# Optimization experiments

Hardware: AMD Instinct MI355X
Metric: run time of the kernel (lower is better)

Reference implementation:

```python
import jax, jax.numpy as jnp
import numpy as np
from jax import lax

LEVEL = 128  # level_num

def _bn(x, g, b, m, v):
    # inference-mode BatchNorm, channel axis = 1
    sh = (1, -1) + (1,) * (x.ndim - 2)
    return (x - m.reshape(sh)) * (g.reshape(sh) * lax.rsqrt(v.reshape(sh) + 1e-5)) + b.reshape(sh)

def _leaky(a):
    return jnp.where(a > 0, a, 0.01 * a)

def _l2n(a):
    return a / jnp.maximum(jnp.linalg.norm(a, axis=1, keepdims=True), 1e-12)

def _resize_bilinear_ac(x, oh, ow):
    # bilinear, align_corners=True, NCHW
    n, c, h, w = x.shape
    ys = jnp.linspace(0.0, h - 1.0, oh)
    xs = jnp.linspace(0.0, w - 1.0, ow)
    y0 = jnp.floor(ys).astype(jnp.int32)
    x0 = jnp.floor(xs).astype(jnp.int32)
    y1 = jnp.minimum(y0 + 1, h - 1)
    x1 = jnp.minimum(x0 + 1, w - 1)
    wy = (ys - y0)[:, None]
    wx = (xs - x0)[None, :]
    Y0, Y1, X0, X1 = y0[:, None], y1[:, None], x0[None, :], x1[None, :]
    return (x[:, :, Y0, X0] * (1 - wy) * (1 - wx) + x[:, :, Y0, X1] * (1 - wy) * wx
            + x[:, :, Y1, X0] * wy * (1 - wx) + x[:, :, Y1, X1] * wy * wx)

def _forward(x, conv1_w, bn1_g, bn1_b, bn1_m, bn1_v, conv2_w, f1_w, f2_w, f2_g, f2_b, f2_m, f2_v,
             out1_w, out1_g, out1_b, out1_m, out1_v, k_w, q_w, v_w, out_w, out_g, out_b, out_m, out_v):
    # conv1: 3x3 conv + BN + LeakyReLU
    y = lax.conv_general_dilated(x, conv1_w, (1, 1), 'SAME', dimension_numbers=('NCHW', 'OIHW', 'NCHW'))
    y = _leaky(_bn(y, bn1_g, bn1_b, bn1_m, bn1_v))
    # conv2: 1x1 conv, 256->128
    x2 = jnp.einsum('nchw,oc->nohw', y, conv2_w)
    N, C, H, W = x2.shape  # C = 128
    x_ave = x2.mean(axis=(2, 3), keepdims=True)  # [N,C,1,1]
    cos = (_l2n(x_ave) * _l2n(x2)).sum(1)        # [N,H,W]
    sh, sw = H // 3, W // 3
    L = sh * sw
    # H,W divisible by 3 -> adaptive_avg_pool2d is identity
    cs = cos.reshape(N, 3, sh, 3, sw).transpose(0, 1, 3, 2, 4).reshape(N, 9, L).transpose(0, 2, 1)  # [N,L,9]
    # LBP bit packing vs center (index 4); weight 0 at index 4 (strict > gives 0 there)
    bits = (cs > cs[:, :, 4:5]).astype(x.dtype)
    wts = jnp.array([1, 2, 4, 8, 0, 16, 32, 64, 128], dtype=x.dtype)
    code = (bits * wts).sum(-1)  # [N,L]
    mn = code.min(-1, keepdims=True)
    mx = code.max(-1, keepdims=True)
    code = (code - mn) / (mx - mn)
    cmin = code.min(-1, keepdims=True)
    cmax = code.max(-1, keepdims=True)
    qlv = (2 * jnp.arange(LEVEL, dtype=x.dtype) + 1) / (2 * LEVEL) * (cmax - cmin) + cmin  # [N,LEVEL]
    inter = (qlv[:, 1] - qlv[:, 0])[:, None, None]  # [N,1,1]
    quant = 1 - jnp.abs(qlv[:, None, :] - code[:, :, None])  # [N,L,LEVEL]
    quant = jnp.where(quant > 1 - inter, quant, 0.0)
    sta = quant.sum(1)                                       # [N,LEVEL]
    sta = sta / sta.sum(-1, keepdims=True)
    sta2 = jnp.stack([qlv, sta], axis=1)                     # [N,2,LEVEL]
    h1 = _leaky(jnp.einsum('ncl,oc->nol', sta2, f1_w))       # f1: 2->64
    h2 = jax.nn.relu(_bn(jnp.einsum('ncl,oc->nol', h1, f2_w), f2_g, f2_b, f2_m, f2_v))  # f2: 64->128
    xa = jnp.broadcast_to(x_ave[:, :, 0, 0][:, :, None], (N, C, LEVEL))
    s = jnp.concatenate([h2, xa], axis=1)                    # [N,256,LEVEL]
    s = jax.nn.relu(_bn(jnp.einsum('ncl,oc->nol', s, out1_w), out1_g, out1_b, out1_m, out1_v))
    k = jnp.einsum('ncl,oc->nol', s, k_w)
    q = jnp.einsum('ncl,oc->nol', s, q_w)
    v = jnp.einsum('ncl,oc->nol', s, v_w)
    w = jax.nn.softmax(jnp.einsum('ncl,ncm->nlm', k, q), axis=-1)  # bmm(k^T, q)
    f = jnp.einsum('nlm,ncm->ncl', w, v)                            # bmm(w, v^T) then transpose
    f = jax.nn.relu(_bn(jnp.einsum('ncl,oc->nol', f, out_w), out_g, out_b, out_m, out_v))
    out = jnp.einsum('ncl,npl->ncp', f, quant).reshape(N, 256, sh, sh)  # bmm(f, quant^T)
    return _resize_bilinear_ac(out, H, W)

def setup_inputs() -> dict:
    key = jax.random.key(0)
    ks = jax.random.split(key, 16)
    f32 = jnp.float32
    def nrm(k, shape, s=0.05):
        return s * jax.random.normal(k, shape, f32)
    def bnp(k, c):
        k1, k2, k3, k4 = jax.random.split(k, 4)
        return (1.0 + 0.1 * jax.random.normal(k1, (c,), f32),
                0.1 * jax.random.normal(k2, (c,), f32),
                0.1 * jax.random.normal(k3, (c,), f32),
                jax.random.uniform(k4, (c,), f32, 0.5, 1.5))
    d = {}
    d['x'] = jax.random.normal(ks[0], (32, 512, 48, 48), f32)
    d['conv1_w'] = nrm(ks[1], (256, 512, 3, 3))
    d['bn1_g'], d['bn1_b'], d['bn1_m'], d['bn1_v'] = bnp(ks[2], 256)
    d['conv2_w'] = nrm(ks[3], (128, 256))
    d['f1_w'] = nrm(ks[4], (64, 2), 0.3)
    d['f2_w'] = nrm(ks[5], (128, 64), 0.1)
    d['f2_g'], d['f2_b'], d['f2_m'], d['f2_v'] = bnp(ks[6], 128)
    d['out1_w'] = nrm(ks[7], (256, 256))
    d['out1_g'], d['out1_b'], d['out1_m'], d['out1_v'] = bnp(ks[8], 256)
    d['k_w'] = nrm(ks[9], (256, 256))
    d['q_w'] = nrm(ks[10], (256, 256))
    d['v_w'] = nrm(ks[11], (256, 256))
    d['out_w'] = nrm(ks[12], (256, 256))
    d['out_g'], d['out_b'], d['out_m'], d['out_v'] = bnp(ks[13], 256)
    return d

def reference(x, conv1_w, bn1_g, bn1_b, bn1_m, bn1_v, conv2_w, f1_w, f2_w, f2_g, f2_b, f2_m, f2_v,
              out1_w, out1_g, out1_b, out1_m, out1_v, k_w, q_w, v_w, out_w, out_g, out_b, out_m, out_v):
    return _forward(x, conv1_w, bn1_g, bn1_b, bn1_m, bn1_v, conv2_w, f1_w, f2_w, f2_g, f2_b, f2_m, f2_v,
                    out1_w, out1_g, out1_b, out1_m, out1_v, k_w, q_w, v_w, out_w, out_g, out_b, out_m, out_v)
```

## Files before the change

kernel.cpp:

```cpp
#include <hip/hip_runtime.h>
#include <math.h>

#define N_IMG 32
#define P2304 2304
#define CIN 512
#define CMID 256
#define C2 128
#define LEV 128

typedef _Float16 half8 __attribute__((ext_vector_type(8)));
typedef float f32x16 __attribute__((ext_vector_type(16)));
typedef unsigned short u16;
typedef unsigned int u32;

__device__ __forceinline__ float wredSum(float v){
#pragma unroll
  for (int o = 32; o > 0; o >>= 1) v += __shfl_down(v, o, 64);
  return v;
}
__device__ __forceinline__ float wredMax(float v){
#pragma unroll
  for (int o = 32; o > 0; o >>= 1) v = fmaxf(v, __shfl_down(v, o, 64));
  return v;
}
__device__ __forceinline__ float wredMin(float v){
#pragma unroll
  for (int o = 32; o > 0; o >>= 1) v = fminf(v, __shfl_down(v, o, 64));
  return v;
}

__device__ __forceinline__ void gll16(const void* g, void* l){
  __builtin_amdgcn_global_load_lds(
      (const __attribute__((address_space(1))) void*)g,
      (__attribute__((address_space(3))) void*)l, 16, 0, 0);
}

__global__ void prep_w1_kernel(const float* __restrict__ w1,
                               uint4* __restrict__ Wh, uint4* __restrict__ Wl){
  int fid = blockIdx.x * 256 + threadIdx.x;
  int lam = fid & 63;
  int c32 = (fid >> 6) & 3;
  int cot = (fid >> 8) & 1;
  int kt  = fid >> 9;
  int co = cot * 128 + c32 * 32 + (lam & 31);
  half8 vh, vl;
#pragma unroll
  for (int j = 0; j < 8; ++j){
    int k = kt * 16 + ((lam >> 5) << 3) + j;
    int r = k >> 9;
    int ci = k & 511;
    float v = w1[co * (CIN * 9) + ci * 9 + r];
    _Float16 h = (_Float16)v;
    vh[j] = h;
    vl[j] = (_Float16)((v - (float)h) * 2048.0f);
  }
  Wh[fid] = *(uint4*)&vh;
  Wl[fid] = *(uint4*)&vl;
}

__global__ void prep_w2_kernel(const float* __restrict__ w2,
                               uint4* __restrict__ Wh, uint4* __restrict__ Wl){
  int fid = blockIdx.x * 256 + threadIdx.x;
  int lam = fid & 63;
  int c32 = (fid >> 6) & 3;
  int kt  = fid >> 8;
  int co = c32 * 32 + (lam & 31);
  half8 vh, vl;
#pragma unroll
  for (int j = 0; j < 8; ++j){
    int k = kt * 16 + ((lam >> 5) << 3) + j;
    float v = w2[co * CMID + k];
    _Float16 h = (_Float16)v;
    vh[j] = h;
    vl[j] = (_Float16)((v - (float)h) * 2048.0f);
  }
  Wh[fid] = *(uint4*)&vh;
  Wl[fid] = *(uint4*)&vl;
}

__global__ void prep_bn_kernel(const float* __restrict__ g1, const float* __restrict__ b1,
                               const float* __restrict__ m1, const float* __restrict__ v1,
                               float* __restrict__ s1, float* __restrict__ t1){
  int c = threadIdx.x;
  float s = g1[c] * (1.0f / sqrtf(v1[c] + 1e-5f));
  s1[c] = s;
  t1[c] = b1[c] - m1[c] * s;
}

__global__ void prep_x_kernel(const float* __restrict__ x,
                              u16* __restrict__ xh, u16* __restrict__ xl,
                              int n0){
  __shared__ float tile[128 * 49];
  const int t = threadIdx.x;
  const int b = blockIdx.x;
  const int n_loc = b / 50;
  const int hp = b - n_loc * 50;
  const int n = n0 + n_loc;
  const int h = hp - 1;
  const bool vrow = (h >= 0) && (h < 48);
  const size_t base_n = (size_t)n_loc * 1280000;
  for (int cc = 0; cc < 4; ++cc){
    if (vrow){
      const float* src = x + (((size_t)n * 512 + cc * 128) * 48 + h) * 48;
#pragma unroll
      for (int i = 0; i < 24; ++i){
        int idx = t + 256 * i;
        int w = idx % 48;
        int c = idx / 48;
        tile[c * 49 + w] = src[(size_t)c * 2304 + w];
      }
    }
    __syncthreads();
    for (int i = 0; i < 13; ++i){
      int idx = t + 256 * i;
      if (idx < 3200){
        int ck_loc = idx / 400;
        int rem = idx - ck_loc * 400;
        int wp = rem >> 3;
        int clp = rem & 7;
        int w = wp - 1;
        int c_loc = ck_loc * 16 + clp * 2;
        float v0 = 0.f, v1 = 0.f;
        if (vrow && (unsigned)w < 48u){
          v0 = tile[c_loc * 49 + w];
          v1 = tile[(c_loc + 1) * 49 + w];
        }
        _Float16 h0 = (_Float16)v0, h1 = (_Float16)v1;
        _Float16 l0 = (_Float16)((v0 - (float)h0) * 2048.0f);
        _Float16 l1 = (_Float16)((v1 - (float)h1) * 2048.0f);
        union { _Float16 hh[2]; u32 uu; } ph, pl;
        ph.hh[0] = h0; ph.hh[1] = h1;
        pl.hh[0] = l0; pl.hh[1] = l1;
        size_t off = base_n + ((size_t)(cc * 8 + ck_loc) * 2500
                               + hp * 50 + wp) * 16 + clp * 2;
        *(u32*)(xh + off) = ph.uu;
        *(u32*)(xl + off) = pl.uu;
      }
    }
    __syncthreads();
  }
}

#define COMPUTE_M(CUR, KF)                                                    \
  {                                                                           \
    const int ct0 = (g & 1) * 2, pt0 = (g >> 1) * 2;                          \
    half8 fAh[2], fAl[2], fBh[2], fBl[2];                                     \
    _Pragma("unroll")                                                         \
    for (int a = 0; a < 2; ++a){                                              \
      fAh[a] = *(half8*)&Abuf[CUR][KF][0][(ct0 + a) * 512 + lam * 8];         \
      fAl[a] = *(half8*)&Abuf[CUR][KF][1][(ct0 + a) * 512 + lam * 8];         \
      fBh[a] = *(half8*)&Bbuf[CUR][KF][0][(pt0 + a) * 512 + lam * 8];         \
      fBl[a] = *(half8*)&Bbuf[CUR][KF][1][(pt0 + a) * 512 + lam * 8];         \
    }                                                                         \
    _Pragma("unroll")                                                         \
    for (int a = 0; a < 2; ++a)                                               \
      _Pragma("unroll")                                                       \
      for (int b = 0; b < 2; ++b){                                            \
        acc_hh[a][b] = __builtin_amdgcn_mfma_f32_32x32x16_f16(                \
            fAh[a], fBh[b], acc_hh[a][b], 0, 0, 0);                           \
        acc_x[a][b] = __builtin_amdgcn_mfma_f32_32x32x16_f16(                 \
            fAh[a], fBl[b], acc_x[a][b], 0, 0, 0);                            \
        acc_x[a][b] = __builtin_amdgcn_mfma_f32_32x32x16_f16(                 \
            fAl[a], fBh[b], acc_x[a][b], 0, 0, 0);                            \
      }                                                                       \
  }

#define WAITV8  asm volatile("s_waitcnt vmcnt(8)"  ::: "memory")
#define WAITV0  asm volatile("s_waitcnt vmcnt(0)"  ::: "memory")
#define BARSB { __builtin_amdgcn_s_barrier(); __builtin_amdgcn_sched_barrier(0); }

template<int NC>
__global__ __launch_bounds__(256, 2) void conv1_lds_kernel(
    const u16* __restrict__ xh, const u16* __restrict__ xl,
    const uint4* __restrict__ Wh, const uint4* __restrict__ Wl,
    const float* __restrict__ s1, const float* __restrict__ t1,
    u16* __restrict__ yh, u16* __restrict__ yl, int n0)
{
  __shared__ _Float16 Abuf[2][2][2][2048];
  __shared__ _Float16 Bbuf[2][2][2][2048];
  const int t = threadIdx.x;
  const int lam = t & 63;
  const int g = t >> 6;

  const int xcd = blockIdx.x & 7;
  const int rest = blockIdx.x >> 3;
  const int NPX = NC / 8;
  const int n_loc = xcd * NPX + rest / 36;
  const int inner = rest % 36;
  const int pt_blk = inner % 18;
  const int cot = inner / 18;
  const int n = n0 + n_loc;

  const int pbase = pt_blk * 128;
  const int khi = lam >> 5;
  const int pp = (g << 5) + (lam & 31);
  const int p = pbase + pp;
  const int ph = p / 48, pw = p - ph * 48;
  const u16* xh_n = xh + (size_t)n_loc * 1280000;
  const u16* xl_n = xl + (size_t)n_loc * 1280000;

  const int S = 144;

  f32x16 acc_hh[2][2], acc_x[2][2];
#pragma unroll
  for (int a = 0; a < 2; ++a)
#pragma unroll
    for (int b = 0; b < 2; ++b){
#pragma unroll
      for (int e = 0; e < 16; ++e){ acc_hh[a][b][e] = 0.f; acc_x[a][b][e] = 0.f; }
    }

#define ISSUE1(SV, BUF)                                                       \
  {                                                                           \
    int s_ = (SV);                                                            \
    int k0_ = 2 * s_;                                                         \
    _Pragma("unroll")                                                         \
    for (int kf = 0; kf < 2; ++kf){                                           \
      int fg_ = ((k0_ + kf) * 2 + cot) * 4 + g;                               \
      gll16(Wh + fg_ * 64 + lam, &Abuf[BUF][kf][0][t * 8]);                   \
      gll16(Wl + fg_ * 64 + lam, &Abuf[BUF][kf][1][t * 8]);                   \
    }                                                                         \
    int r_ = k0_ >> 5;                                          \
    int ck0_ = k0_ & 31;                         \
    int qpp_ = (ph + r_ / 3) * 50 + (pw + r_ % 3);            \
    _Pragma("unroll")                                                         \
    for (int kf = 0; kf < 2; ++kf){                                           \
      size_t o_ = ((size_t)(ck0_ + kf) * 2500 + qpp_) * 16 + (khi << 3);      \
      gll16(xh_n + o_, &Bbuf[BUF][kf][0][t * 8]);                             \
      gll16(xl_n + o_, &Bbuf[BUF][kf][1][t * 8]);                             \
    }                                                                         \
  }

  ISSUE1(0, 0);
  ISSUE1(1, 1);

  for (int s = 0; s < S - 1; ++s){
    WAITV8;
    BARSB;
    __builtin_amdgcn_s_setprio(1);
    COMPUTE_M(s & 1, 0);
    COMPUTE_M(s & 1, 1);
    __builtin_amdgcn_s_setprio(0);
    if (s + 2 < S){
      BARSB;
      ISSUE1(s + 2, s & 1);
    }
  }
  WAITV0;
  BARSB;
  __builtin_amdgcn_s_setprio(1);
  COMPUTE_M((S - 1) & 1, 0);
  COMPUTE_M((S - 1) & 1, 1);
  __builtin_amdgcn_s_setprio(0);
#undef ISSUE1

  const int cobase = cot * 128;
#pragma unroll
  for (int a = 0; a < 2; ++a){
    const int ctile = (g & 1) * 2 + a;
#pragma unroll
    for (int b = 0; b < 2; ++b){
      const int ptile = (g >> 1) * 2 + b;
      const int pg = pbase + ptile * 32 + (lam & 31);
#pragma unroll
      for (int q = 0; q < 4; ++q){
        const int co0 = cobase + ctile * 32 + 8 * q + 4 * khi;
        const int co16 = co0 >> 4, col = co0 & 15;
        union { _Float16 h[4]; uint2 u; } Uh, Ul;
#pragma unroll
        for (int i = 0; i < 4; ++i){
          const int rg = 4 * q + i;
          const int co = co0 + i;
          float val = acc_hh[a][b][rg] + acc_x[a][b][rg] * (1.0f / 2048.0f);
          val = val * s1[co] + t1[co];
          val = val > 0.f ? val : 0.01f * val;
          _Float16 h = (_Float16)val;
          Uh.h[i] = h;
          Ul.h[i] = (_Float16)((val - (float)h) * 2048.0f);
        }
        size_t off = (((size_t)n * 16 + co16) * P2304 + pg) * 16 + col;
        *(uint2*)(yh + off) = Uh.u;
        *(uint2*)(yl + off) = Ul.u;
      }
    }
  }
}

__global__ __launch_bounds__(256, 2) void conv2_lds_kernel(
    const u16* __restrict__ yh, const u16* __restrict__ yl,
    const uint4* __restrict__ Wh, const uint4* __restrict__ Wl,
    float* __restrict__ out)
{
  __shared__ _Float16 Abuf[2][2][2][2048];
  __shared__ _Float16 Bbuf[2][2][2][2048];
  const int t = threadIdx.x;
  const int lam = t & 63;
  const int g = t >> 6;

  const int pt_blk = blockIdx.x % 18;
  const int n = blockIdx.x / 18;
  const int pbase = pt_blk * 128;
  const int khi = lam >> 5;
  const int p = pbase + (g << 5) + (lam & 31);
  const u16* yh_n = yh + (size_t)n * 589824;
  const u16* yl_n = yl + (size_t)n * 589824;

  const int S = 8;

  f32x16 acc_hh[2][2], acc_x[2][2];
#pragma unroll
  for (int a = 0; a < 2; ++a)
#pragma unroll
    for (int b = 0; b < 2; ++b){
#pragma unroll
      for (int e = 0; e < 16; ++e){ acc_hh[a][b][e] = 0.f; acc_x[a][b][e] = 0.f; }
    }

#define ISSUE2(SV, BUF)                                                       \
  {                                                                           \
    int s_ = (SV);                                                            \
    int k0_ = 2 * s_;                                                         \
    _Pragma("unroll")                                                         \
    for (int kf = 0; kf < 2; ++kf){                                           \
      int fg_ = (k0_ + kf) * 4 + g;                                           \
      gll16(Wh + fg_ * 64 + lam, &Abuf[BUF][kf][0][t * 8]);                   \
      gll16(Wl + fg_ * 64 + lam, &Abuf[BUF][kf][1][t * 8]);                   \
    }                                                                         \
    _Pragma("unroll")                                                         \
    for (int kf = 0; kf < 2; ++kf){                                           \
      size_t o_ = ((size_t)(k0_ + kf) * P2304 + p) * 16 + (khi << 3);         \
      gll16(yh_n + o_, &Bbuf[BUF][kf][0][t * 8]);                             \
      gll16(yl_n + o_, &Bbuf[BUF][kf][1][t * 8]);                             \
    }                                                                         \
  }

  ISSUE2(0, 0);
  ISSUE2(1, 1);

  for (int s = 0; s < S - 1; ++s){
    WAITV8;
    BARSB;
    __builtin_amdgcn_s_setprio(1);
    COMPUTE_M(s & 1, 0);
    COMPUTE_M(s & 1, 1);
    __builtin_amdgcn_s_setprio(0);
    if (s + 2 < S){
      BARSB;
      ISSUE2(s + 2, s & 1);
    }
  }
  WAITV0;
  BARSB;
  __builtin_amdgcn_s_setprio(1);
  COMPUTE_M((S - 1) & 1, 0);
  COMPUTE_M((S - 1) & 1, 1);
  __builtin_amdgcn_s_setprio(0);
#undef ISSUE2

#pragma unroll
  for (int a = 0; a < 2; ++a){
    const int ctile = (g & 1) * 2 + a;
#pragma unroll
    for (int b = 0; b < 2; ++b){
      const int ptile = (g >> 1) * 2 + b;
      const int pg = pbase + ptile * 32 + (lam & 31);
#pragma unroll
      for (int rg = 0; rg < 16; ++rg){
        const int row = (rg & 3) + 8 * (rg >> 2) + 4 * khi;
        const int co = ctile * 32 + row;
        float val = acc_hh[a][b][rg] + acc_x[a][b][rg] * (1.0f / 2048.0f);
        out[((size_t)n * C2 + co) * P2304 + pg] = val;
      }
    }
  }
}

template<int R, int CPT, int COTN, bool BN>
__global__ __launch_bounds__(256, 2) void conv_mfma_kernel(
    const float* __restrict__ in, const uint4* __restrict__ Wh, const uint4* __restrict__ Wl,
    const float* __restrict__ s1, const float* __restrict__ t1, float* __restrict__ out)
{
  __shared__ _Float16 Abuf[2][2][2][2048];
  __shared__ _Float16 Bbuf[2][2][2][2048];
  const int t = threadIdx.x;
  const int lam = t & 63;
  const int g = t >> 6;

  int n, pt_blk, cot;
  if (COTN == 2){
    int xcd = blockIdx.x & 7;
    int rest = blockIdx.x >> 3;
    n = xcd * 4 + rest / 36;
    int inner = rest % 36;
    pt_blk = inner % 18;
    cot = inner / 18;
  } else {
    pt_blk = blockIdx.x % 18;
    cot = 0;
    n = blockIdx.x / 18;
  }
  const int pbase = pt_blk * 128;
  const int cobase = cot * 128;

  const int khi = lam >> 5;
  const int pp = (g << 5) + (lam & 31);
  const int p = pbase + pp;
  const int ph = p / 48, pw = p - ph * 48;
  const float* in_n = in + (size_t)n * CPT * P2304;

  const int S = (R * CPT) / 32;
  const int KTPT = CPT / 16;

  f32x16 acc_hh[2][2], acc_x[2][2];
#pragma unroll
  for (int a = 0; a < 2; ++a)
#pragma unroll
    for (int b = 0; b < 2; ++b){
#pragma unroll
      for (int e = 0; e < 16; ++e){ acc_hh[a][b][e] = 0.f; acc_x[a][b][e] = 0.f; }
    }

  uint4 rAh[2], rAl[2];
  float rB[16];
  bool vmask;

#define ISSUE(SV)                                                             \
  {                                                                           \
    int s_ = (SV);                                                            \
    _Pragma("unroll")                                                         \
    for (int kf = 0; kf < 2; ++kf){                                           \
      int fi = (((2 * s_ + kf) * COTN + cot) * 4 + g) * 64 + lam;             \
      rAh[kf] = Wh[fi];                                                       \
      rAl[kf] = Wl[fi];                                                       \
    }                                                                         \
    int r_ = (R == 1) ? 0 : ((2 * s_) / KTPT);                                \
    int cbase_ = ((2 * s_) % KTPT) * 16;                                      \
    int dh_ = (R == 1) ? 0 : (r_ / 3 - 1);                                    \
    int dw_ = (R == 1) ? 0 : (r_ - (r_ / 3) * 3 - 1);                         \
    int hh_ = ph + dh_, ww_ = pw + dw_;                                       \
    vmask = ((unsigned)hh_ < 48u) & ((unsigned)ww_ < 48u);                    \
    int hc_ = min(max(hh_, 0), 47), wc_ = min(max(ww_, 0), 47);               \
    const float* src_ = in_n + hc_ * 48 + wc_                                 \
                        + (size_t)(cbase_ + khi * 8) * P2304;                 \
    _Pragma("unroll")                                                         \
    for (int kf = 0; kf < 2; ++kf)                                            \
      _Pragma("unroll")                                                       \
      for (int j = 0; j < 8; ++j)                                             \
        rB[kf * 8 + j] = src_[(kf * 16 + j) * P2304];                         \
  }

#define STASH(NXT)                                                            \
  {                                                                           \
    _Pragma("unroll")                                                         \
    for (int kf = 0; kf < 2; ++kf){                                           \
      *(uint4*)&Abuf[NXT][kf][0][t * 8] = rAh[kf];                            \
      *(uint4*)&Abuf[NXT][kf][1][t * 8] = rAl[kf];                            \
      half8 vh, vl;                                                           \
      _Pragma("unroll")                                                       \
      for (int j = 0; j < 8; ++j){                                            \
        float v = vmask ? rB[kf * 8 + j] : 0.0f;                              \
        _Float16 h = (_Float16)v;                                             \
        vh[j] = h;                                                            \
        vl[j] = (_Float16)((v - (float)h) * 2048.0f);                         \
      }                                                                       \
      *(half8*)&Bbuf[NXT][kf][0][t * 8] = vh;                                 \
      *(half8*)&Bbuf[NXT][kf][1][t * 8] = vl;                                 \
    }                                                                         \
  }

  ISSUE(0);
  STASH(0);
  __syncthreads();

  for (int s = 0; s < S; ++s){
    const int cur = s & 1, nxt = cur ^ 1;
    const bool more = (s + 1 < S);
    if (more) ISSUE(s + 1);
    COMPUTE_M(cur, 0);
    if (more) STASH(nxt);
    COMPUTE_M(cur, 1);
    __syncthreads();
  }
#undef ISSUE
#undef STASH

  const int M = COTN * 128;
#pragma unroll
  for (int a = 0; a < 2; ++a){
    const int ctile = (g & 1) * 2 + a;
#pragma unroll
    for (int b = 0; b < 2; ++b){
      const int ptile = (g >> 1) * 2 + b;
      const int pg = pbase + ptile * 32 + (lam & 31);
#pragma unroll
      for (int rg = 0; rg < 16; ++rg){
        const int row = (rg & 3) + 8 * (rg >> 2) + 4 * (lam >> 5);
        const int co = cobase + ctile * 32 + row;
        float val = acc_hh[a][b][rg] + acc_x[a][b][rg] * (1.0f / 2048.0f);
        if (BN){
          val = val * s1[co] + t1[co];
          val = val > 0.f ? val : 0.01f * val;
        }
        out[((size_t)n * M + co) * P2304 + pg] = val;
      }
    }
  }
}

__global__ void xave_kernel(const float* __restrict__ x2, float* __restrict__ xave){
  __shared__ float red[4];
  int nc = blockIdx.x, t = threadIdx.x;
  const float* row = x2 + nc * P2304;
  float s = 0.f;
#pragma unroll
  for (int i = 0; i < 9; i++) s += row[t + 256 * i];
  float w = wredSum(s);
  if ((t & 63) == 0) red[t >> 6] = w;
  __syncthreads();
  if (t == 0) xave[nc] = (red[0] + red[1] + red[2] + red[3]) * (1.0f / 2304.0f);
}

__global__ void xan_kernel(const float* __restrict__ xave, float* __restrict__ xan){
  __shared__ float red[2];
  int n = blockIdx.x, t = threadIdx.x;
  float v = xave[n * 128 + t];
  float w = wredSum(v * v);
  if ((t & 63) == 0) red[t >> 6] = w;
  __syncthreads();
  float norm = fmaxf(sqrtf(red[0] + red[1]), 1e-12f);
  xan[n * 128 + t] = v / norm;
}

__global__ void cos_kernel(const float* __restrict__ x2, const float* __restrict__ xan,
                           float* __restrict__ cosb){
  int idx = blockIdx.x * 256 + threadIdx.x;
  if (idx >= N_IMG * P2304) return;
  int n = idx / P2304;
  int p = idx - n * P2304;
  const float* xp = x2 + n * C2 * P2304 + p;
  const float* an = xan + n * 128;
  float dot = 0.f, ss = 0.f;
  for (int c = 0; c < 128; c++){
    float v = xp[c * P2304];
    dot += an[c] * v;
    ss  += v * v;
  }
  cosb[idx] = dot / fmaxf(sqrtf(ss), 1e-12f);
}

__global__ void lbp_kernel(const float* __restrict__ cosb, float* __restrict__ code,
                           float* __restrict__ qlv){
  __shared__ float red[4];
  int n = blockIdx.x;
  int l = threadIdx.x;
  int ir = l >> 4, ic = l & 15;
  const float* cn = cosb + n * P2304;
  float cs4 = cn[(16 + ir) * 48 + (16 + ic)];
  const float wts[9] = {1.f, 2.f, 4.f, 8.f, 0.f, 16.f, 32.f, 64.f, 128.f};
  float codev = 0.f;
#pragma unroll
  for (int j = 0; j < 9; j++){
    int jr = j / 3, jc = j - 3 * (j / 3);
    float vv = cn[(jr * 16 + ir) * 48 + (jc * 16 + ic)];
    if (vv > cs4) codev += wts[j];
  }
  float w;
  w = wredMin(codev);
  if ((l & 63) == 0) red[l >> 6] = w;
  __syncthreads();
  float mn = fminf(fminf(red[0], red[1]), fminf(red[2], red[3]));
  __syncthreads();
  w = wredMax(codev);
  if ((l & 63) == 0) red[l >> 6] = w;
  __syncthreads();
  float mx = fmaxf(fmaxf(red[0], red[1]), fmaxf(red[2], red[3]));
  __syncthreads();
  float cd = (codev - mn) / (mx - mn);
  w = wredMin(cd);
  if ((l & 63) == 0) red[l >> 6] = w;
  __syncthreads();
  float cmin = fminf(fminf(red[0], red[1]), fminf(red[2], red[3]));
  __syncthreads();
  w = wredMax(cd);
  if ((l & 63) == 0) red[l >> 6] = w;
  __syncthreads();
  float cmax = fmaxf(fmaxf(red[0], red[1]), fmaxf(red[2], red[3]));
  code[n * 256 + l] = cd;
  if (l < 128){
    float tmp = (float)(2 * l + 1) * (1.0f / 256.0f);
    qlv[n * 128 + l] = tmp * (cmax - cmin) + cmin;
  }
}

__global__ void quant_kernel(const float* __restrict__ code, const float* __restrict__ qlv,
                             float* __restrict__ quantT){
  __shared__ float cs[256];
  __shared__ float qs[128];
  int n = blockIdx.x, t = threadIdx.x;
  cs[t] = code[n * 256 + t];
  if (t < 128) qs[t] = qlv[n * 128 + t];
  __syncthreads();
  float thr = 1.0f - (qs[1] - qs[0]);
  float* dst = quantT + n * LEV * 256;
#pragma unroll 4
  for (int i = 0; i < 128; i++){
    int v = t + 256 * i;
    int lv = v >> 8;
    int p = v & 255;
    float qq = 1.0f - fabsf(qs[lv] - cs[p]);
    dst[v] = (qq > thr) ? qq : 0.f;
  }
}

__global__ void sta_rows_kernel(const float* __restrict__ quantT, float* __restrict__ raw){
  int b = blockIdx.x;
  int t = threadIdx.x;
  int n = b >> 5;
  int row = (b & 31) * 4 + (t >> 6);
  int lane = t & 63;
  const float* src = quantT + ((size_t)(n * LEV + row)) * 256 + lane * 4;
  float4 v = *(const float4*)src;
  float s = v.x + v.y + v.z + v.w;
  s = wredSum(s);
  if (lane == 0) raw[n * 128 + row] = s;
}

__global__ void sta_norm_kernel(const float* __restrict__ raw, float* __restrict__ sta){
  __shared__ float red[2];
  int n = blockIdx.x, t = threadIdx.x;
  float v = raw[n * 128 + t];
  float w = wredSum(v);
  if ((t & 63) == 0) red[t >> 6] = w;
  __syncthreads();
  sta[n * 128 + t] = v / (red[0] + red[1]);
}

__global__ void h1_kernel(const float* __restrict__ f1w, const float* __restrict__ qlv,
                          const float* __restrict__ sta, float* __restrict__ h1){
  int idx = blockIdx.x * 256 + threadIdx.x;
  if (idx >= N_IMG * 64 * 128) return;
  int l = idx & 127;
  int n = idx >> 13;
  int o = (idx >> 7) & 63;
  float a = f1w[o * 2] * qlv[n * 128 + l] + f1w[o * 2 + 1] * sta[n * 128 + l];
  h1[idx] = a > 0.f ? a : 0.01f * a;
}

__global__ void gemm_w_kernel(const float* __restrict__ Wm, const float* __restrict__ B,
                              float* __restrict__ Cout, int Cdim, int O, int total, int mode,
                              const float* __restrict__ g, const float* __restrict__ bb,
                              const float* __restrict__ mm, const float* __restrict__ vv){
  int idx = blockIdx.x * 256 + threadIdx.x;
  if (idx >= total) return;
  int per_n = (O >> 2) << 7;
  int n = idx / per_n;
  int rem = idx - n * per_n;
  int o0 = (rem >> 7) << 2;
  int l = rem & 127;
  const float* Bn = B + (n * Cdim) * 128 + l;
  const float* w0 = Wm + (o0 + 0) * Cdim;
  const float* w1 = Wm + (o0 + 1) * Cdim;
  const float* w2 = Wm + (o0 + 2) * Cdim;
  const float* w3 = Wm + (o0 + 3) * Cdim;
  float a0 = 0, a1 = 0, a2 = 0, a3 = 0;
  for (int c = 0; c < Cdim; c++){
    float bv = Bn[c * 128];
    a0 += w0[c] * bv; a1 += w1[c] * bv; a2 += w2[c] * bv; a3 += w3[c] * bv;
  }
  float av[4] = {a0, a1, a2, a3};
#pragma unroll
  for (int j = 0; j < 4; j++){
    int o = o0 + j;
    float val = av[j];
    if (mode == 1){
      float s = g[o] * (1.0f / sqrtf(vv[o] + 1e-5f));
      val = (val - mm[o]) * s + bb[o];
      val = fmaxf(val, 0.f);
    }
    Cout[(n * O + o) * 128 + l] = val;
  }
}

__global__ void gemm_kqv_kernel(const float* __restrict__ kW, const float* __restrict__ qW,
                                const float* __restrict__ vW, const float* __restrict__ B,
                                float* __restrict__ kO, float* __restrict__ qO,
                                float* __restrict__ vO){
  int idx = blockIdx.x * 256 + threadIdx.x;
  int sel = idx >> 18;
  int rem = idx & 262143;
  const float* Wm = (sel == 0) ? kW : (sel == 1) ? qW : vW;
  float* Cout     = (sel == 0) ? kO : (sel == 1) ? qO : vO;
  int n = rem >> 13;
  int r2 = rem & 8191;
  int o0 = (r2 >> 7) << 2;
  int l = r2 & 127;
  const float* Bn = B + (n * 256) * 128 + l;
  const float* w0 = Wm + (o0 + 0) * 256;
  const float* w1 = Wm + (o0 + 1) * 256;
  const float* w2 = Wm + (o0 + 2) * 256;
  const float* w3 = Wm + (o0 + 3) * 256;
  float a0 = 0, a1 = 0, a2 = 0, a3 = 0;
  for (int c = 0; c < 256; c++){
    float bv = Bn[c * 128];
    a0 += w0[c] * bv; a1 += w1[c] * bv; a2 += w2[c] * bv; a3 += w3[c] * bv;
  }
  float* dst = Cout + (n * 256 + o0) * 128 + l;
  dst[0] = a0; dst[128] = a1; dst[256] = a2; dst[384] = a3;
}

__global__ void concat_kernel(const float* __restrict__ h2, const float* __restrict__ xave,
                              float* __restrict__ s){
  int idx = blockIdx.x * 256 + threadIdx.x;
  if (idx >= N_IMG * 256 * 128) return;
  int l = idx & 127;
  int c = (idx >> 7) & 255;
  int n = idx >> 15;
  s[idx] = (c < 128) ? h2[(n * 128 + c) * 128 + l] : xave[n * 128 + (c - 128)];
}

__global__ void attn_sc_kernel(const float* __restrict__ k, const float* __restrict__ q,
                               float* __restrict__ sc){
  int idx = blockIdx.x * 256 + threadIdx.x;
  if (idx >= N_IMG * 32 * 128) return;
  int m = idx & 127;
  int l0 = ((idx >> 7) & 31) << 2;
  int n = idx >> 12;
  const float* kn = k + n * 256 * 128;
  const float* qn = q + n * 256 * 128 + m;
  float a0 = 0, a1 = 0, a2 = 0, a3 = 0;
  for (int c = 0; c < 256; c++){
    float qv = qn[c * 128];
    const float* kr = kn + c * 128 + l0;
    a0 += kr[0] * qv; a1 += kr[1] * qv; a2 += kr[2] * qv; a3 += kr[3] * qv;
  }
  float* dst = sc + (n * 128 + l0) * 128 + m;
  dst[0] = a0; dst[128] = a1; dst[256] = a2; dst[384] = a3;
}

__global__ void softmax_kernel(float* __restrict__ sc){
  __shared__ float red[2];
  int row = blockIdx.x;
  int t = threadIdx.x;
  float v = sc[row * 128 + t];
  float w = wredMax(v);
  if ((t & 63) == 0) red[t >> 6] = w;
  __syncthreads();
  float mx = fmaxf(red[0], red[1]);
  float e = expf(v - mx);
  float s = wredSum(e);
  __syncthreads();
  if ((t & 63) == 0) red[t >> 6] = s;
  __syncthreads();
  sc[row * 128 + t] = e / (red[0] + red[1]);
}

__global__ void transpose_sc_kernel(const float* __restrict__ sc, float* __restrict__ scT){
  int idx = blockIdx.x * 256 + threadIdx.x;
  if (idx >= N_IMG * 128 * 128) return;
  int l = idx & 127;
  int m = (idx >> 7) & 127;
  int n = idx >> 14;
  scT[idx] = sc[(n * 128 + l) * 128 + m];
}

__global__ void attn_f_kernel(const float* __restrict__ vb, const float* __restrict__ scT,
                              float* __restrict__ f){
  int idx = blockIdx.x * 256 + threadIdx.x;
  if (idx >= N_IMG * 64 * 128) return;
  int l = idx & 127;
  int c0 = ((idx >> 7) & 63) << 2;
  int n = idx >> 13;
  const float* vn = vb + (n * 256 + c0) * 128;
  const float* sn = scT + n * 128 * 128 + l;
  float a0 = 0, a1 = 0, a2 = 0, a3 = 0;
  for (int m = 0; m < 128; m++){
    float sv = sn[m * 128];
    a0 += vn[m] * sv; a1 += vn[128 + m] * sv; a2 += vn[256 + m] * sv; a3 += vn[384 + m] * sv;
  }
  float* dst = f + (n * 256 + c0) * 128 + l;
  dst[0] = a0; dst[128] = a1; dst[256] = a2; dst[384] = a3;
}

__global__ void final_kernel(const float* __restrict__ g, const float* __restrict__ quantT,
                             float* __restrict__ outs){
  int idx = blockIdx.x * 256 + threadIdx.x;
  if (idx >= N_IMG * 64 * 256) return;
  int p = idx & 255;
  int c0 = ((idx >> 8) & 63) << 2;
  int n = idx >> 14;
  const float* gn = g + (n * 256 + c0) * 128;
  const float* qn = quantT + (n * LEV) * 256 + p;
  float a0 = 0, a1 = 0, a2 = 0, a3 = 0;
  for (int lv = 0; lv < 128; lv++){
    float qv = qn[lv * 256];
    a0 += gn[lv] * qv; a1 += gn[128 + lv] * qv; a2 += gn[256 + lv] * qv; a3 += gn[384 + lv] * qv;
  }
  float* dst = outs + (n * 256 + c0) * 256 + p;
  dst[0] = a0; dst[256] = a1; dst[512] = a2; dst[768] = a3;
}

__global__ void resize_kernel(const float* __restrict__ outs, float* __restrict__ dout){
  int idx = blockIdx.x * 256 + threadIdx.x;
  if (idx >= N_IMG * 256 * P2304) return;
  int ow = idx % 48;
  int tmp = idx / 48;
  int oh = tmp % 48;
  int nc = tmp / 48;
  const float* src = outs + nc * 256;
  float fy = oh * (15.0f / 47.0f);
  float fx = ow * (15.0f / 47.0f);
  int y0 = (int)fy;
  int x0 = (int)fx;
  int y1 = min(y0 + 1, 15);
  int x1 = min(x0 + 1, 15);
  float wy = fy - (float)y0;
  float wx = fx - (float)x0;
  float v00 = src[y0 * 16 + x0], v01 = src[y0 * 16 + x1];
  float v10 = src[y1 * 16 + x0], v11 = src[y1 * 16 + x1];
  dout[idx] = v00 * (1.f - wy) * (1.f - wx) + v01 * (1.f - wy) * wx
            + v10 * wy * (1.f - wx) + v11 * wy * wx;
}

extern "C" void kernel_launch(void* const* d_in, const int* in_sizes, int n_in,
                              void* d_out, int out_size, void* d_ws, size_t ws_size,
                              hipStream_t stream)
{
  const float* x       = (const float*)d_in[0];
  const float* conv1_w = (const float*)d_in[1];
  const float* bn1_g   = (const float*)d_in[2];
  const float* bn1_b   = (const float*)d_in[3];
  const float* bn1_m   = (const float*)d_in[4];
  const float* bn1_v   = (const float*)d_in[5];
  const float* conv2_w = (const float*)d_in[6];
  const float* f1_w    = (const float*)d_in[7];
  const float* f2_w    = (const float*)d_in[8];
  const float* f2_g    = (const float*)d_in[9];
  const float* f2_b    = (const float*)d_in[10];
  const float* f2_m    = (const float*)d_in[11];
  const float* f2_v    = (const float*)d_in[12];
  const float* out1_w  = (const float*)d_in[13];
  const float* out1_g  = (const float*)d_in[14];
  const float* out1_b  = (const float*)d_in[15];
  const float* out1_m  = (const float*)d_in[16];
  const float* out1_v  = (const float*)d_in[17];
  const float* k_w     = (const float*)d_in[18];
  const float* q_w     = (const float*)d_in[19];
  const float* v_w     = (const float*)d_in[20];
  const float* out_w   = (const float*)d_in[21];
  const float* out_g   = (const float*)d_in[22];
  const float* out_b   = (const float*)d_in[23];
  const float* out_m   = (const float*)d_in[24];
  const float* out_v   = (const float*)d_in[25];

  float* ws = (float*)d_ws;
  float* dout = (float*)d_out;

  float* w_y   = ws;
  float* w_x2  = ws + 18874368;
  float* w_W1h = ws + 28311552;
  float* w_W1l = ws + 28901376;
  float* w_W2h = ws + 29491200;
  float* w_W2l = ws + 29507584;
  float* w_s1  = ws + 29523968;
  float* w_t1  = ws + 29524224;
  float* w_xave = w_y + 0;
  float* w_xan  = w_y + 4096;
  float* w_cos  = w_y + 8192;
  float* w_code = w_y + 81920;
  float* w_qlv  = w_y + 90112;
  float* w_sta  = w_y + 94208;
  float* w_quant= w_y + 98304;
  float* w_h1   = w_y + 1146880;
  float* w_h2   = w_y + 1409024;
  float* w_s    = w_y + 1933312;
  float* w_k    = w_y + 2981888;
  float* w_q    = w_y + 4030464;
  float* w_v    = w_y + 5079040;
  float* w_sc   = w_y + 6127616;
  float* w_scT  = w_y + 6651904;
  float* w_f    = w_y + 7176192;
  float* w_g    = w_y + 8224768;
  float* w_outs = w_y + 9273344;
  float* w_s2   = w_y + 11370496;
  float* w_raw  = w_y + 12419072;

  prep_w1_kernel<<<576, 256, 0, stream>>>(conv1_w, (uint4*)w_W1h, (uint4*)w_W1l);
  prep_w2_kernel<<<16, 256, 0, stream>>>(conv2_w, (uint4*)w_W2h, (uint4*)w_W2l);
  prep_bn_kernel<<<1, 256, 0, stream>>>(bn1_g, bn1_b, bn1_m, bn1_v, w_s1, w_t1);

  const size_t BASE_F = 29524480;
  const size_t XPI_F  = 640000;
  const size_t ws_f = ws_size / 4;
  int NCc = 0;
  if (ws_f >= BASE_F + 2 * 32 * XPI_F)      NCc = 32;
  else if (ws_f >= BASE_F + 2 * 16 * XPI_F) NCc = 16;

  if (NCc > 0){
    u16* w_xh = (u16*)(ws + BASE_F);
    u16* w_xl = w_xh + (size_t)NCc * 1280000;
    u16* w_yh = (u16*)w_y;
    u16* w_yl = (u16*)(w_y + 9437184);
    const int nchunk = N_IMG / NCc;
    for (int c = 0; c < nchunk; ++c){
      int n0 = c * NCc;
      prep_x_kernel<<<NCc * 50, 256, 0, stream>>>(x, w_xh, w_xl, n0);
      if (NCc == 32)
        conv1_lds_kernel<32><<<1152, 256, 0, stream>>>(
            w_xh, w_xl, (const uint4*)w_W1h, (const uint4*)w_W1l, w_s1, w_t1,
            w_yh, w_yl, n0);
      else
        conv1_lds_kernel<16><<<576, 256, 0, stream>>>(
            w_xh, w_xl, (const uint4*)w_W1h, (const uint4*)w_W1l, w_s1, w_t1,
            w_yh, w_yl, n0);
    }
    conv2_lds_kernel<<<576, 256, 0, stream>>>(
        w_yh, w_yl, (const uint4*)w_W2h, (const uint4*)w_W2l, w_x2);
  } else {
    conv_mfma_kernel<9, 512, 2, true><<<1152, 256, 0, stream>>>(
        x, (const uint4*)w_W1h, (const uint4*)w_W1l, w_s1, w_t1, w_y);
    conv_mfma_kernel<1, 256, 1, false><<<576, 256, 0, stream>>>(
        w_y, (const uint4*)w_W2h, (const uint4*)w_W2l, w_s1, w_t1, w_x2);
  }

  xave_kernel<<<4096, 256, 0, stream>>>(w_x2, w_xave);
  xan_kernel<<<32, 128, 0, stream>>>(w_xave, w_xan);
  cos_kernel<<<288, 256, 0, stream>>>(w_x2, w_xan, w_cos);
  lbp_kernel<<<32, 256, 0, stream>>>(w_cos, w_code, w_qlv);
  quant_kernel<<<32, 256, 0, stream>>>(w_code, w_qlv, w_quant);
  sta_rows_kernel<<<1024, 256, 0, stream>>>(w_quant, w_raw);
  sta_norm_kernel<<<32, 128, 0, stream>>>(w_raw, w_sta);
  h1_kernel<<<1024, 256, 0, stream>>>(f1_w, w_qlv, w_sta, w_h1);
  gemm_w_kernel<<<512, 256, 0, stream>>>(f2_w, w_h1, w_h2, 64, 128, N_IMG * 32 * 128, 1,
                                         f2_g, f2_b, f2_m, f2_v);
  concat_kernel<<<4096, 256, 0, stream>>>(w_h2, w_xave, w_s);
  gemm_w_kernel<<<1024, 256, 0, stream>>>(out1_w, w_s, w_s2, 256, 256, N_IMG * 64 * 128, 1,
                                          out1_g, out1_b, out1_m, out1_v);
  gemm_kqv_kernel<<<3072, 256, 0, stream>>>(k_w, q_w, v_w, w_s2, w_k, w_q, w_v);
  attn_sc_kernel<<<512, 256, 0, stream>>>(w_k, w_q, w_sc);
  softmax_kernel<<<4096, 128, 0, stream>>>(w_sc);
  transpose_sc_kernel<<<2048, 256, 0, stream>>>(w_sc, w_scT);
  attn_f_kernel<<<1024, 256, 0, stream>>>(w_v, w_scT, w_f);
  gemm_w_kernel<<<1024, 256, 0, stream>>>(out_w, w_f, w_g, 256, 256, N_IMG * 64 * 128, 1,
                                          out_g, out_b, out_m, out_v);
  final_kernel<<<2048, 256, 0, stream>>>(w_g, w_quant, w_outs);
  resize_kernel<<<73728, 256, 0, stream>>>(w_outs, dout);
}
```

Before: 1.496 ms.

## Widen conv1 blocks to 512 threads sharing weight tiles across 256 pixels

Replaces the 256-thread conv1 kernel with a 512-thread variant in which each block covers 256 output pixels instead of 128. The 128-channel weight tile in LDS is now loaded cooperatively and reused by twice as many pixels. This halves the weight traffic per output and halves the grid size. In exchange, occupancy drops to one block per launch bound, there are fewer blocks to spread across CUs, and the barriers span more waves.

```diff
diff --git a/kernel.cpp b/kernel.cpp
--- a/kernel.cpp
+++ b/kernel.cpp
@@ -141,9 +141,80 @@
   }
 }
 
-#define COMPUTE_M(CUR, KF)                                                    \
+#define WAITV8  asm volatile("s_waitcnt vmcnt(8)"  ::: "memory")
+#define WAITV6  asm volatile("s_waitcnt vmcnt(6)"  ::: "memory")
+#define WAITV0  asm volatile("s_waitcnt vmcnt(0)"  ::: "memory")
+#define BARSB { __builtin_amdgcn_s_barrier(); __builtin_amdgcn_sched_barrier(0); }
+
+template<int NC>
+__global__ __launch_bounds__(512, 1) void conv1_wide_kernel(
+    const u16* __restrict__ xh, const u16* __restrict__ xl,
+    const uint4* __restrict__ Wh, const uint4* __restrict__ Wl,
+    const float* __restrict__ s1, const float* __restrict__ t1,
+    u16* __restrict__ yh, u16* __restrict__ yl, int n0)
+{
+  __shared__ _Float16 Abuf[2][2][2][2048];
+  __shared__ _Float16 Bbuf[2][2][2][4096];
+  const int t = threadIdx.x;
+  const int lam = t & 63;
+  const int wid = t >> 6;
+  const int cg = wid & 1;
+  const int pgw = wid >> 1;
+
+  const int xcd = blockIdx.x & 7;
+  const int rest = blockIdx.x >> 3;
+  const int n_loc = xcd * (NC / 8) + rest / 18;
+  const int inner = rest % 18;
+  const int pt = inner % 9;
+  const int cot = inner / 9;
+  const int n = n0 + n_loc;
+
+  const int pbase = pt * 256;
+  const int khi = lam >> 5;
+  const int ps = pbase + wid * 32 + (lam & 31);
+  const int phb = ps / 48, pwb = ps - (ps / 48) * 48;
+  const u16* xh_n = xh + (size_t)n_loc * 1280000;
+  const u16* xl_n = xl + (size_t)n_loc * 1280000;
+
+  const int S = 144;
+
+  f32x16 acc_hh[2][2], acc_x[2][2];
+#pragma unroll
+  for (int a = 0; a < 2; ++a)
+#pragma unroll
+    for (int b = 0; b < 2; ++b){
+#pragma unroll
+      for (int e = 0; e < 16; ++e){ acc_hh[a][b][e] = 0.f; acc_x[a][b][e] = 0.f; }
+    }
+
+#define ISSUE_W(SV, BUF)                                                      \
   {                                                                           \
-    const int ct0 = (g & 1) * 2, pt0 = (g >> 1) * 2;                          \
+    int s_ = (SV);                                                            \
+    int k0_ = 2 * s_;                                                         \
+    _Pragma("unroll")                                                         \
+    for (int i = 0; i < 2; ++i){                                              \
+      int a_ = wid * 2 + i;                             \
+      int c32_ = a_ & 3;                                                      \
+      int kf_ = (a_ >> 2) & 1;                                                \
+      int hl_ = (a_ >> 3) & 1;                                                \
+      int fg_ = ((k0_ + kf_) * 2 + cot) * 4 + c32_;                           \
+      const uint4* sw_ = (hl_ ? Wl : Wh) + fg_ * 64 + lam;                    \
+      gll16(sw_, &Abuf[BUF][kf_][hl_][c32_ * 512 + lam * 8]);                 \
+    }                                                                         \
+    int r_ = k0_ >> 5;                                          \
+    int ck0_ = k0_ & 31;                         \
+    int qpp_ = (phb + r_ / 3) * 50 + (pwb + r_ % 3);                          \
+    _Pragma("unroll")                                                         \
+    for (int kf = 0; kf < 2; ++kf){                                           \
+      size_t o_ = ((size_t)(ck0_ + kf) * 2500 + qpp_) * 16 + (khi << 3);      \
+      gll16(xh_n + o_, &Bbuf[BUF][kf][0][wid * 512 + lam * 8]);               \
+      gll16(xl_n + o_, &Bbuf[BUF][kf][1][wid * 512 + lam * 8]);               \
+    }                                                                         \
+  }
+
+#define COMPUTE_W(CUR, KF)                                                    \
+  {                                                                           \
+    const int ct0 = cg * 2, pt0 = pgw * 2;                                    \
     half8 fAh[2], fAl[2], fBh[2], fBl[2];                                     \
     _Pragma("unroll")                                                         \
     for (int a = 0; a < 2; ++a){                                              \
@@ -165,106 +236,31 @@
       }                                                                       \
   }
 
-#define WAITV8  asm volatile("s_waitcnt vmcnt(8)"  ::: "memory")
-#define WAITV0  asm volatile("s_waitcnt vmcnt(0)"  ::: "memory")
-#define BARSB { __builtin_amdgcn_s_barrier(); __builtin_amdgcn_sched_barrier(0); }
-
-template<int NC>
-__global__ __launch_bounds__(256, 2) void conv1_lds_kernel(
-    const u16* __restrict__ xh, const u16* __restrict__ xl,
-    const uint4* __restrict__ Wh, const uint4* __restrict__ Wl,
-    const float* __restrict__ s1, const float* __restrict__ t1,
-    u16* __restrict__ yh, u16* __restrict__ yl, int n0)
-{
-  __shared__ _Float16 Abuf[2][2][2][2048];
-  __shared__ _Float16 Bbuf[2][2][2][2048];
-  const int t = threadIdx.x;
-  const int lam = t & 63;
-  const int g = t >> 6;
-
-  const int xcd = blockIdx.x & 7;
-  const int rest = blockIdx.x >> 3;
-  const int NPX = NC / 8;
-  const int n_loc = xcd * NPX + rest / 36;
-  const int inner = rest % 36;
-  const int pt_blk = inner % 18;
-  const int cot = inner / 18;
-  const int n = n0 + n_loc;
-
-  const int pbase = pt_blk * 128;
-  const int khi = lam >> 5;
-  const int pp = (g << 5) + (lam & 31);
-  const int p = pbase + pp;
-  const int ph = p / 48, pw = p - ph * 48;
-  const u16* xh_n = xh + (size_t)n_loc * 1280000;
-  const u16* xl_n = xl + (size_t)n_loc * 1280000;
-
-  const int S = 144;
-
-  f32x16 acc_hh[2][2], acc_x[2][2];
-#pragma unroll
-  for (int a = 0; a < 2; ++a)
-#pragma unroll
-    for (int b = 0; b < 2; ++b){
-#pragma unroll
-      for (int e = 0; e < 16; ++e){ acc_hh[a][b][e] = 0.f; acc_x[a][b][e] = 0.f; }
-    }
-
-#define ISSUE1(SV, BUF)                                                       \
-  {                                                                           \
-    int s_ = (SV);                                                            \
-    int k0_ = 2 * s_;                                                         \
-    _Pragma("unroll")                                                         \
-    for (int kf = 0; kf < 2; ++kf){                                           \
-      int fg_ = ((k0_ + kf) * 2 + cot) * 4 + g;                               \
-      gll16(Wh + fg_ * 64 + lam, &Abuf[BUF][kf][0][t * 8]);                   \
-      gll16(Wl + fg_ * 64 + lam, &Abuf[BUF][kf][1][t * 8]);                   \
-    }                                                                         \
-    int r_ = k0_ >> 5;                                          \
-    int ck0_ = k0_ & 31;                         \
-    int qpp_ = (ph + r_ / 3) * 50 + (pw + r_ % 3);            \
-    _Pragma("unroll")                                                         \
-    for (int kf = 0; kf < 2; ++kf){                                           \
-      size_t o_ = ((size_t)(ck0_ + kf) * 2500 + qpp_) * 16 + (khi << 3);      \
-      gll16(xh_n + o_, &Bbuf[BUF][kf][0][t * 8]);                             \
-      gll16(xl_n + o_, &Bbuf[BUF][kf][1][t * 8]);                             \
-    }                                                                         \
-  }
-
-  ISSUE1(0, 0);
-  ISSUE1(1, 1);
-
-  for (int s = 0; s < S - 1; ++s){
-    WAITV8;
+  ISSUE_W(0, 0);
+  ISSUE_W(1, 1);
+
+  for (int s = 0; s < S; ++s){
+    if (s < S - 1) { WAITV6; } else { WAITV0; }
     BARSB;
     __builtin_amdgcn_s_setprio(1);
-    COMPUTE_M(s & 1, 0);
-    COMPUTE_M(s & 1, 1);
+    COMPUTE_W(s & 1, 0);
+    COMPUTE_W(s & 1, 1);
     __builtin_amdgcn_s_setprio(0);
-    if (s + 2 < S){
-      BARSB;
-      ISSUE1(s + 2, s & 1);
-    }
-  }
-  WAITV0;
-  BARSB;
-  __builtin_amdgcn_s_setprio(1);
-  COMPUTE_M((S - 1) & 1, 0);
-  COMPUTE_M((S - 1) & 1, 1);
-  __builtin_amdgcn_s_setprio(0);
-#undef ISSUE1
-
-  const int cobase = cot * 128;
+    BARSB;
+    if (s + 2 < S) ISSUE_W(s + 2, s & 1);
+  }
+#undef ISSUE_W
+#undef COMPUTE_W
+
+  const int cobase = cot * 128 + cg * 64;
 #pragma unroll
   for (int a = 0; a < 2; ++a){
-    const int ctile = (g & 1) * 2 + a;
 #pragma unroll
     for (int b = 0; b < 2; ++b){
-      const int ptile = (g >> 1) * 2 + b;
-      const int pg = pbase + ptile * 32 + (lam & 31);
+      const int pg = pbase + (pgw * 2 + b) * 32 + (lam & 31);
 #pragma unroll
       for (int q = 0; q < 4; ++q){
-        const int co0 = cobase + ctile * 32 + 8 * q + 4 * khi;
+        const int co0 = cobase + a * 32 + 8 * q + 4 * khi;
         const int co16 = co0 >> 4, col = co0 & 15;
         union { _Float16 h[4]; uint2 u; } Uh, Ul;
 #pragma unroll
@@ -285,6 +281,30 @@
     }
   }
 }
+
+#define COMPUTE_M(CUR, KF)                                                    \
+  {                                                                           \
+    const int ct0 = (g & 1) * 2, pt0 = (g >> 1) * 2;                          \
+    half8 fAh[2], fAl[2], fBh[2], fBl[2];                                     \
+    _Pragma("unroll")                                                         \
+    for (int a = 0; a < 2; ++a){                                              \
+      fAh[a] = *(half8*)&Abuf[CUR][KF][0][(ct0 + a) * 512 + lam * 8];         \
+      fAl[a] = *(half8*)&Abuf[CUR][KF][1][(ct0 + a) * 512 + lam * 8];         \
+      fBh[a] = *(half8*)&Bbuf[CUR][KF][0][(pt0 + a) * 512 + lam * 8];         \
+      fBl[a] = *(half8*)&Bbuf[CUR][KF][1][(pt0 + a) * 512 + lam * 8];         \
+    }                                                                         \
+    _Pragma("unroll")                                                         \
+    for (int a = 0; a < 2; ++a)                                               \
+      _Pragma("unroll")                                                       \
+      for (int b = 0; b < 2; ++b){                                            \
+        acc_hh[a][b] = __builtin_amdgcn_mfma_f32_32x32x16_f16(                \
+            fAh[a], fBh[b], acc_hh[a][b], 0, 0, 0);                           \
+        acc_x[a][b] = __builtin_amdgcn_mfma_f32_32x32x16_f16(                 \
+            fAh[a], fBl[b], acc_x[a][b], 0, 0, 0);                            \
+        acc_x[a][b] = __builtin_amdgcn_mfma_f32_32x32x16_f16(                 \
+            fAl[a], fBh[b], acc_x[a][b], 0, 0, 0);                            \
+      }                                                                       \
+  }
 
 __global__ __launch_bounds__(256, 2) void conv2_lds_kernel(
     const u16* __restrict__ yh, const u16* __restrict__ yl,
@@ -905,11 +925,11 @@
       int n0 = c * NCc;
       prep_x_kernel<<<NCc * 50, 256, 0, stream>>>(x, w_xh, w_xl, n0);
       if (NCc == 32)
-        conv1_lds_kernel<32><<<1152, 256, 0, stream>>>(
+        conv1_wide_kernel<32><<<576, 512, 0, stream>>>(
             w_xh, w_xl, (const uint4*)w_W1h, (const uint4*)w_W1l, w_s1, w_t1,
             w_yh, w_yl, n0);
       else
-        conv1_lds_kernel<16><<<576, 256, 0, stream>>>(
+        conv1_wide_kernel<16><<<288, 512, 0, stream>>>(
             w_xh, w_xl, (const uint4*)w_W1h, (const uint4*)w_W1l, w_s1, w_t1,
             w_yh, w_yl, n0);
     }
```

After: 1.587 ms. 1.06x slower.

## Fuse small post-conv stages: h1 into f2 GEMM, concat into out1, scores+softmax+transpose

Applied to the files above, without the earlier changes.

Computes the f1 projection and LeakyReLU inline inside the f2 GEMM, and reads h2 and the broadcast x_ave directly in the out1 GEMM so the concat buffer is gone. The attention score, softmax and transpose are merged into one kernel that reduces each row across the block and writes the transposed probabilities directly. This removes several launches and intermediate global round trips. In exchange, the f1 math is recomputed per output group, and the fused kernel writes scT with strided stores.

```diff
diff --git a/kernel.cpp b/kernel.cpp
--- a/kernel.cpp
+++ b/kernel.cpp
@@ -635,15 +635,72 @@
   sta[n * 128 + t] = v / (red[0] + red[1]);
 }
 
-__global__ void h1_kernel(const float* __restrict__ f1w, const float* __restrict__ qlv,
-                          const float* __restrict__ sta, float* __restrict__ h1){
+__global__ void h2_fused_kernel(const float* __restrict__ f1w, const float* __restrict__ f2w,
+                                const float* __restrict__ qlv, const float* __restrict__ sta,
+                                const float* __restrict__ g, const float* __restrict__ bb,
+                                const float* __restrict__ mm, const float* __restrict__ vv,
+                                float* __restrict__ h2){
+  int idx = blockIdx.x * 256 + threadIdx.x;
+  if (idx >= N_IMG * 32 * 128) return;
+  int l = idx & 127;
+  int o0 = ((idx >> 7) & 31) << 2;
+  int n = idx >> 12;
+  float qv = qlv[n * 128 + l];
+  float sv = sta[n * 128 + l];
+  const float* w0 = f2w + (o0 + 0) * 64;
+  const float* w1 = f2w + (o0 + 1) * 64;
+  const float* w2 = f2w + (o0 + 2) * 64;
+  const float* w3 = f2w + (o0 + 3) * 64;
+  float a0 = 0, a1 = 0, a2 = 0, a3 = 0;
+  for (int c = 0; c < 64; c++){
+    float hv = f1w[2 * c] * qv + f1w[2 * c + 1] * sv;
+    hv = hv > 0.f ? hv : 0.01f * hv;
+    a0 += w0[c] * hv; a1 += w1[c] * hv; a2 += w2[c] * hv; a3 += w3[c] * hv;
+  }
+  float av[4] = {a0, a1, a2, a3};
+#pragma unroll
+  for (int j = 0; j < 4; j++){
+    int o = o0 + j;
+    float s = g[o] * (1.0f / sqrtf(vv[o] + 1e-5f));
+    float val = (av[j] - mm[o]) * s + bb[o];
+    h2[(n * 128 + o) * 128 + l] = fmaxf(val, 0.f);
+  }
+}
+
+__global__ void out1_fused_kernel(const float* __restrict__ Wm, const float* __restrict__ h2,
+                                  const float* __restrict__ xave,
+                                  const float* __restrict__ g, const float* __restrict__ bb,
+                                  const float* __restrict__ mm, const float* __restrict__ vv,
+                                  float* __restrict__ s2){
   int idx = blockIdx.x * 256 + threadIdx.x;
   if (idx >= N_IMG * 64 * 128) return;
   int l = idx & 127;
+  int o0 = ((idx >> 7) & 63) << 2;
   int n = idx >> 13;
-  int o = (idx >> 7) & 63;
-  float a = f1w[o * 2] * qlv[n * 128 + l] + f1w[o * 2 + 1] * sta[n * 128 + l];
-  h1[idx] = a > 0.f ? a : 0.01f * a;
+  const float* h2n = h2 + (n * 128) * 128 + l;
+  const float* xa = xave + n * 128;
+  const float* w0 = Wm + (o0 + 0) * 256;
+  const float* w1 = Wm + (o0 + 1) * 256;
+  const float* w2 = Wm + (o0 + 2) * 256;
+  const float* w3 = Wm + (o0 + 3) * 256;
+  float a0 = 0, a1 = 0, a2 = 0, a3 = 0;
+  for (int c = 0; c < 128; c++){
+    float bv = h2n[c * 128];
+    a0 += w0[c] * bv; a1 += w1[c] * bv; a2 += w2[c] * bv; a3 += w3[c] * bv;
+  }
+  for (int c = 0; c < 128; c++){
+    float bv = xa[c];
+    a0 += w0[128 + c] * bv; a1 += w1[128 + c] * bv;
+    a2 += w2[128 + c] * bv; a3 += w3[128 + c] * bv;
+  }
+  float av[4] = {a0, a1, a2, a3};
+#pragma unroll
+  for (int j = 0; j < 4; j++){
+    int o = o0 + j;
+    float s = g[o] * (1.0f / sqrtf(vv[o] + 1e-5f));
+    float val = (av[j] - mm[o]) * s + bb[o];
+    s2[(n * 256 + o) * 128 + l] = fmaxf(val, 0.f);
+  }
 }
 
 __global__ void gemm_w_kernel(const float* __restrict__ Wm, const float* __restrict__ B,
@@ -708,23 +765,18 @@
   dst[0] = a0; dst[128] = a1; dst[256] = a2; dst[384] = a3;
 }
 
-__global__ void concat_kernel(const float* __restrict__ h2, const float* __restrict__ xave,
-                              float* __restrict__ s){
-  int idx = blockIdx.x * 256 + threadIdx.x;
-  if (idx >= N_IMG * 256 * 128) return;
-  int l = idx & 127;
-  int c = (idx >> 7) & 255;
-  int n = idx >> 15;
-  s[idx] = (c < 128) ? h2[(n * 128 + c) * 128 + l] : xave[n * 128 + (c - 128)];
-}
-
-__global__ void attn_sc_kernel(const float* __restrict__ k, const float* __restrict__ q,
-                               float* __restrict__ sc){
-  int idx = blockIdx.x * 256 + threadIdx.x;
-  if (idx >= N_IMG * 32 * 128) return;
-  int m = idx & 127;
-  int l0 = ((idx >> 7) & 31) << 2;
-  int n = idx >> 12;
+__global__ void attn_scsm_kernel(const float* __restrict__ k, const float* __restrict__ q,
+                                 float* __restrict__ scT){
+  __shared__ float redm[2][2][4];
+  __shared__ float reds[2][2][4];
+  int b = blockIdx.x;
+  int t = threadIdx.x;
+  int n = b >> 4;
+  int h = t >> 7;
+  int wv = (t >> 6) & 1;
+  int lane = t & 63;
+  int m = t & 127;
+  int l0 = (((b & 15) * 2 + h)) * 4;
   const float* kn = k + n * 256 * 128;
   const float* qn = q + n * 256 * 128 + m;
   float a0 = 0, a1 = 0, a2 = 0, a3 = 0;
@@ -733,34 +785,27 @@
     const float* kr = kn + c * 128 + l0;
     a0 += kr[0] * qv; a1 += kr[1] * qv; a2 += kr[2] * qv; a3 += kr[3] * qv;
   }
-  float* dst = sc + (n * 128 + l0) * 128 + m;
-  dst[0] = a0; dst[128] = a1; dst[256] = a2; dst[384] = a3;
-}
-
-__global__ void softmax_kernel(float* __restrict__ sc){
-  __shared__ float red[2];
-  int row = blockIdx.x;
-  int t = threadIdx.x;
-  float v = sc[row * 128 + t];
-  float w = wredMax(v);
-  if ((t & 63) == 0) red[t >> 6] = w;
-  __syncthreads();
-  float mx = fmaxf(red[0], red[1]);
-  float e = expf(v - mx);
-  float s = wredSum(e);
-  __syncthreads();
-  if ((t & 63) == 0) red[t >> 6] = s;
-  __syncthreads();
-  sc[row * 128 + t] = e / (red[0] + red[1]);
-}
-
-__global__ void transpose_sc_kernel(const float* __restrict__ sc, float* __restrict__ scT){
-  int idx = blockIdx.x * 256 + threadIdx.x;
-  if (idx >= N_IMG * 128 * 128) return;
-  int l = idx & 127;
-  int m = (idx >> 7) & 127;
-  int n = idx >> 14;
-  scT[idx] = sc[(n * 128 + l) * 128 + m];
+  float av[4] = {a0, a1, a2, a3};
+#pragma unroll
+  for (int r = 0; r < 4; r++){
+    float w = wredMax(av[r]);
+    if (lane == 0) redm[h][wv][r] = w;
+  }
+  __syncthreads();
+  float ex[4];
+#pragma unroll
+  for (int r = 0; r < 4; r++){
+    float mx = fmaxf(redm[h][0][r], redm[h][1][r]);
+    ex[r] = expf(av[r] - mx);
+    float s = wredSum(ex[r]);
+    if (lane == 0) reds[h][wv][r] = s;
+  }
+  __syncthreads();
+  float* dst = scT + n * 16384 + m * 128 + l0;
+#pragma unroll
+  for (int r = 0; r < 4; r++){
+    dst[r] = ex[r] / (reds[h][0][r] + reds[h][1][r]);
+  }
 }
 
 __global__ void attn_f_kernel(const float* __restrict__ vb, const float* __restrict__ scT,
@@ -870,13 +915,10 @@
   float* w_qlv  = w_y + 90112;
   float* w_sta  = w_y + 94208;
   float* w_quant= w_y + 98304;
-  float* w_h1   = w_y + 1146880;
   float* w_h2   = w_y + 1409024;
-  float* w_s    = w_y + 1933312;
   float* w_k    = w_y + 2981888;
   float* w_q    = w_y + 4030464;
   float* w_v    = w_y + 5079040;
-  float* w_sc   = w_y + 6127616;
   float* w_scT  = w_y + 6651904;
   float* w_f    = w_y + 7176192;
   float* w_g    = w_y + 8224768;
@@ -929,16 +971,12 @@
   quant_kernel<<<32, 256, 0, stream>>>(w_code, w_qlv, w_quant);
   sta_rows_kernel<<<1024, 256, 0, stream>>>(w_quant, w_raw);
   sta_norm_kernel<<<32, 128, 0, stream>>>(w_raw, w_sta);
-  h1_kernel<<<1024, 256, 0, stream>>>(f1_w, w_qlv, w_sta, w_h1);
-  gemm_w_kernel<<<512, 256, 0, stream>>>(f2_w, w_h1, w_h2, 64, 128, N_IMG * 32 * 128, 1,
-                                         f2_g, f2_b, f2_m, f2_v);
-  concat_kernel<<<4096, 256, 0, stream>>>(w_h2, w_xave, w_s);
-  gemm_w_kernel<<<1024, 256, 0, stream>>>(out1_w, w_s, w_s2, 256, 256, N_IMG * 64 * 128, 1,
-                                          out1_g, out1_b, out1_m, out1_v);
+  h2_fused_kernel<<<512, 256, 0, stream>>>(f1_w, f2_w, w_qlv, w_sta,
+                                           f2_g, f2_b, f2_m, f2_v, w_h2);
+  out1_fused_kernel<<<1024, 256, 0, stream>>>(out1_w, w_h2, w_xave,
+                                              out1_g, out1_b, out1_m, out1_v, w_s2);
   gemm_kqv_kernel<<<3072, 256, 0, stream>>>(k_w, q_w, v_w, w_s2, w_k, w_q, w_v);
-  attn_sc_kernel<<<512, 256, 0, stream>>>(w_k, w_q, w_sc);
-  softmax_kernel<<<4096, 128, 0, stream>>>(w_sc);
-  transpose_sc_kernel<<<2048, 256, 0, stream>>>(w_sc, w_scT);
+  attn_scsm_kernel<<<512, 256, 0, stream>>>(w_k, w_q, w_scT);
   attn_f_kernel<<<1024, 256, 0, stream>>>(w_v, w_scT, w_f);
   gemm_w_kernel<<<1024, 256, 0, stream>>>(out_w, w_f, w_g, 256, 256, N_IMG * 64 * 128, 1,
                                           out_g, out_b, out_m, out_v);
```

After: 1.485 ms. No clear change (-0.7%).
